# Optimization experiments

Measured on AMD Instinct MI355X. Metric: run time of the kernel, lower is better.

Reference implementation:

```python
import jax, jax.numpy as jnp
import numpy as np

B, L_PREM, T_HYP, D = 32, 256, 128, 256


def setup_inputs() -> dict:
    key = jax.random.key(0)
    ks = jax.random.split(key, 6)
    scale = 1.0 / np.sqrt(D)
    return {
        "x": jax.random.normal(ks[0], (B, L_PREM + T_HYP, D), dtype=jnp.float32),
        "w_y": jax.random.normal(ks[1], (D, D), dtype=jnp.float32) * scale,
        "w_h": jax.random.normal(ks[2], (D, D), dtype=jnp.float32) * scale,
        "w_r": jax.random.normal(ks[3], (D, D), dtype=jnp.float32) * scale,
        "w_alpha": jax.random.normal(ks[4], (D, 1), dtype=jnp.float32) * scale,
        "w_t": jax.random.normal(ks[5], (D, D), dtype=jnp.float32) * scale,
        "L": L_PREM,
    }


def reference(x, w_y, w_h, w_r, w_alpha, w_t, L):
    # x: (B, L + T, D)
    premise = x[:, :L, :]                 # Y: (B, L, D)
    hypothesis = jnp.swapaxes(x[:, L:, :], 0, 1)  # (T, B, D)

    # Y @ W_y does not depend on t: hoist out of the scan (same math).
    WY = jnp.einsum("bld,de->ble", premise, w_y)  # (B, L, D)

    def step(r_tm1, h_t):
        # r_tm1: (B, D), h_t: (B, D)
        s = h_t @ w_h + r_tm1 @ w_r                 # (B, D)
        Mt = jnp.tanh(WY + s[:, None, :])           # (B, L, D)
        scores = jnp.squeeze(Mt @ w_alpha, -1)      # (B, L)
        alpha = jax.nn.softmax(scores, axis=-1)     # (B, L)
        r_t = jnp.einsum("bl,bld->bd", alpha, premise) + r_tm1 @ w_t
        return r_t, r_t

    r0 = jnp.zeros_like(premise[:, 0, :])           # (B, D)
    _, rs = jax.lax.scan(step, r0, hypothesis)      # rs: (T, B, D)
    return jnp.swapaxes(rs, 0, 1)                   # (B, T, D)
```

## Files before the change

kernel.cpp:

```cpp
#include <hip/hip_runtime.h>
#include <hip/hip_fp16.h>

typedef unsigned long long u64;

#define C2X 2.8853900817779268f
#define LOG2E 1.4426950408889634f

#define WYS_OFF   0u
#define PR_OFF    4194304u
#define PREMH_OFF 8388608u
#define HWH_OFF   12582912u
#define WTH_OFF   16777216u
#define WTR_OFF   16908288u
#define ZP_OFF    17039360u
#define RCH_OFF   18087936u
#define MEMSET_SZ 1179648u

#define PRC_OFF   0u
#define WTRC_OFF  16384u
#define PREMC_OFF 32768u
#define WTC_OFF   49152u
#define WYC_OFF   65536u
#define HWHC_OFF  81920u
#define SCH_OFF   98304u
#define WACH_OFF  98432u
#define AL_OFF    98560u
#define RB_OFF    99584u
#define PART_OFF  100608u
#define RED_OFF   104832u
#define LDS_TOTAL 104864u

__global__ __launch_bounds__(256) void prep_all(const float* __restrict__ x,
                                                const float* __restrict__ wy,
                                                const float* __restrict__ wh,
                                                const float* __restrict__ wr,
                                                const float* __restrict__ wt,
                                                __half* __restrict__ wys,
                                                __half* __restrict__ prh,
                                                float* __restrict__ hwh,
                                                __half* __restrict__ wtrh,
                                                __half* __restrict__ premh,
                                                __half* __restrict__ wth) {
    const int blk = blockIdx.x;
    if (blk >= 1568) {
        int i = (blk - 1568) * 256 + threadIdx.x;
        float4 v; __half* dst; int e;
        if (i < 524288) {
            e = i * 4; int b = e >> 16;
            v = *(const float4*)(x + (size_t)e + (size_t)b * 32768);
            dst = premh + e;
        } else if (i < 540672) {
            e = (i - 524288) * 4;
            v = *(const float4*)(wt + e);
            dst = wth + e;
        } else return;
        __half h[4] = {__float2half(v.x),__float2half(v.y),__float2half(v.z),__float2half(v.w)};
        *(uint2*)dst = *(const uint2*)h;
        return;
    }
    __shared__ float At[8][256];
    const int d = threadIdx.x;
    int mode, row0;
    if (blk < 1024)      { mode = 0; row0 = blk * 8; }
    else if (blk < 1536) { mode = 1; row0 = (blk - 1024) * 8; }
    else                 { mode = 2; row0 = (blk - 1536) * 8; }
    for (int rr = 0; rr < 8; ++rr) {
        int r = row0 + rr;
        const float* src;
        if (mode == 0)      { int b = r >> 8, l = r & 255; src = x + (size_t)(b * 384 + l) * 256; }
        else if (mode == 1) { int tt = r >> 5, bb = r & 31; src = x + (size_t)(bb * 384 + 256 + tt) * 256; }
        else                { src = wt + (size_t)r * 256; }
        At[rr][d] = src[d];
    }
    __syncthreads();
    if (mode == 0) {
        float accy[8] = {0,0,0,0,0,0,0,0}, accr[8] = {0,0,0,0,0,0,0,0};
        for (int k = 0; k < 256; k += 2) {
            float y0 = wy[(size_t)k * 256 + d], y1 = wy[(size_t)(k + 1) * 256 + d];
            float r0 = wr[(size_t)k * 256 + d], r1 = wr[(size_t)(k + 1) * 256 + d];
#pragma unroll
            for (int rr = 0; rr < 8; ++rr) {
                float2 a = *(const float2*)&At[rr][k];
                accy[rr] = fmaf(a.x, y0, accy[rr]); accy[rr] = fmaf(a.y, y1, accy[rr]);
                accr[rr] = fmaf(a.x, r0, accr[rr]); accr[rr] = fmaf(a.y, r1, accr[rr]);
            }
        }
        for (int rr = 0; rr < 8; ++rr) {
            int r = row0 + rr;
            wys[(size_t)r * 256 + d] = __float2half(accy[rr] * C2X);
            prh[(size_t)r * 256 + d] = __float2half(accr[rr]);
        }
    } else {
        const float* w = (mode == 1) ? wh : wr;
        float acc[8] = {0,0,0,0,0,0,0,0};
        for (int k = 0; k < 256; k += 4) {
            float w0 = w[(size_t)k * 256 + d], w1 = w[(size_t)(k+1) * 256 + d];
            float w2 = w[(size_t)(k+2) * 256 + d], w3 = w[(size_t)(k+3) * 256 + d];
#pragma unroll
            for (int rr = 0; rr < 8; ++rr) {
                float4 a = *(const float4*)&At[rr][k];
                float t0 = fmaf(a.x, w0, acc[rr]);
                t0 = fmaf(a.y, w1, t0);
                t0 = fmaf(a.z, w2, t0);
                acc[rr] = fmaf(a.w, w3, t0);
            }
        }
        for (int rr = 0; rr < 8; ++rr) {
            int r = row0 + rr;
            if (mode == 1) hwh[(size_t)r * 256 + d] = acc[rr] * C2X;
            else           wtrh[(size_t)r * 256 + d] = __float2half(acc[rr]);
        }
    }
}

__device__ __forceinline__ u64 agent_load64(const u64* p) {
    return __hip_atomic_load(p, __ATOMIC_RELAXED, __HIP_MEMORY_SCOPE_AGENT);
}
__device__ __forceinline__ void agent_store64(u64* p, u64 v) {
    __hip_atomic_store(p, v, __ATOMIC_RELAXED, __HIP_MEMORY_SCOPE_AGENT);
}

__global__ __launch_bounds__(512, 1) void wbw_main(
    const __half* __restrict__ wys, const __half* __restrict__ prh,
    const __half* __restrict__ premh, const __half* __restrict__ wth,
    const __half* __restrict__ wtrh, const float* __restrict__ hwh,
    const float* __restrict__ walpha, float* __restrict__ out,
    u64* __restrict__ zp, u64* __restrict__ rch)
{
    extern __shared__ char lds[];
    const int tid = threadIdx.x;
    const int b = blockIdx.x >> 3, j = blockIdx.x & 7;

    float* hwhc  = (float*)(lds + HWHC_OFF);
    float* s_ch  = (float*)(lds + SCH_OFF);
    float* wa_ch = (float*)(lds + WACH_OFF);
    float* al    = (float*)(lds + AL_OFF);
    float* rb    = (float*)(lds + RB_OFF);
    float* part  = (float*)(lds + PART_OFF);
    float* red   = (float*)(lds + RED_OFF);

    {
        const int prt = tid & 3;
        for (int it = 0; it < 2; ++it) {
            int row = it * 128 + (tid >> 2);
            size_t g = (size_t)row * 256 + j * 32 + prt * 8;
            unsigned lo = (unsigned)row * 64 + (unsigned)prt * 16;
            *(uint4*)(lds + PRC_OFF   + lo) = *(const uint4*)(prh   + (size_t)b * 65536 + g);
            *(uint4*)(lds + WTRC_OFF  + lo) = *(const uint4*)(wtrh  + g);
            *(uint4*)(lds + PREMC_OFF + lo) = *(const uint4*)(premh + (size_t)b * 65536 + g);
            *(uint4*)(lds + WTC_OFF   + lo) = *(const uint4*)(wth   + g);
            *(uint4*)(lds + WYC_OFF   + lo) = *(const uint4*)(wys   + (size_t)b * 65536 + g);
        }
    }
    for (int it = 0; it < 8; ++it) {
        int idx = it * 512 + tid;
        int tt = idx >> 5, dd = idx & 31;
        hwhc[idx] = hwh[((size_t)tt * 32 + b) * 256 + j * 32 + dd];
    }
    if (tid < 32) wa_ch[tid] = walpha[j * 32 + tid] * (-2.0f * LOG2E);
    if (tid < 256) { al[tid] = 0.f; rb[tid] = 0.f; }
    if (tid < 8)   red[tid] = (tid == 0 || tid == 4) ? 1.f : 0.f;
    __syncthreads();

    for (int t = 0; t <= 128; ++t) {
        const int par = t & 1;
        if (t < 128) {
            {
                const int half_ = tid >> 8;
                const int s16 = (tid >> 4) & 15;
                const int d0 = (tid & 15) * 2;
                const __half* mat = (const __half*)(lds + (half_ ? WTRC_OFF : PRC_OFF));
                const float* vec = half_ ? rb : al;
                float ax = 0.f, ay = 0.f;
#pragma unroll
                for (int i = 0; i < 16; ++i) {
                    int l = s16 + i * 16;
                    float v = vec[l];
                    float2 mf = __half22float2(*(const __half2*)&mat[l * 32 + d0]);
                    ax = fmaf(v, mf.x, ax); ay = fmaf(v, mf.y, ay);
                }
                const int row = half_ * 16 + s16;
                part[row * 33 + d0] = ax; part[row * 33 + d0 + 1] = ay;
            }
            __syncthreads();
            if (tid < 32) {
                const float* rd = red + (par ^ 1) * 4;
                float rD = __builtin_amdgcn_rcpf(rd[0] + rd[1] + rd[2] + rd[3]);
                float se = 0.f, sr = 0.f;
#pragma unroll
                for (int s2 = 0; s2 < 16; ++s2) {
                    se += part[s2 * 33 + tid];
                    sr += part[(16 + s2) * 33 + tid];
                }
                s_ch[tid] = fmaf(fmaf(se, rD, sr), C2X, hwhc[t * 32 + tid]);
            }
            __syncthreads();
            {
                const int l = tid >> 1, dh = (tid & 1) << 4;
                union { uint4 u[2]; __half h[16]; } W;
                W.u[0] = *(const uint4*)(lds + WYC_OFF + (unsigned)l * 64 + (unsigned)dh * 2);
                W.u[1] = *(const uint4*)(lds + WYC_OFF + (unsigned)l * 64 + (unsigned)dh * 2 + 16);
                float acc = 0.f;
#pragma unroll
                for (int i = 0; i < 16; ++i) {
                    float arg = __half2float(W.h[i]) + s_ch[dh + i];
                    float u = __builtin_amdgcn_rcpf(__builtin_amdgcn_exp2f(arg) + 1.f);
                    acc = fmaf(wa_ch[dh + i], u, acc);
                }
                acc += __shfl_xor(acc, 1, 64);
                if ((tid & 1) == 0) {
                    u64 pk = ((u64)(unsigned)(t + 1) << 32) | (u64)__float_as_uint(acc);
                    agent_store64(&zp[(size_t)((par * 32 + b) * 8 + j) * 256 + l], pk);
                }
            }
        }
        {
            const int half_ = tid >> 8;
            const int s16 = (tid >> 4) & 15;
            const int d0 = (tid & 15) * 2;
            const __half* mat = (const __half*)(lds + (half_ ? WTC_OFF : PREMC_OFF));
            const float* vec = half_ ? rb : al;
            float ax = 0.f, ay = 0.f;
#pragma unroll
            for (int i = 0; i < 16; ++i) {
                int l = s16 + i * 16;
                float v = vec[l];
                float2 mf = __half22float2(*(const __half2*)&mat[l * 32 + d0]);
                ax = fmaf(v, mf.x, ax); ay = fmaf(v, mf.y, ay);
            }
            const int row = half_ * 16 + s16;
            part[row * 33 + d0] = ax; part[row * 33 + d0 + 1] = ay;
        }
        __syncthreads();
        if (tid >= 448 && tid < 480) {
            const int d = tid - 448;
            const float* rd = red + (par ^ 1) * 4;
            float rD = __builtin_amdgcn_rcpf(rd[0] + rd[1] + rd[2] + rd[3]);
            float se = 0.f, sr = 0.f;
#pragma unroll
            for (int s2 = 0; s2 < 16; ++s2) {
                se += part[s2 * 33 + d];
                sr += part[(16 + s2) * 33 + d];
            }
            float rv = fmaf(se, rD, sr);
            if (t >= 1) out[((size_t)b * 128 + (t - 1)) * 256 + j * 32 + d] = rv;
            if (t < 128) {
                u64 pk = ((u64)(unsigned)t << 32) | (u64)__float_as_uint(rv);
                agent_store64(&rch[(size_t)(par * 32 + b) * 256 + j * 32 + d], pk);
            }
        } else if (tid < 256 && t < 128) {
            const u64* zb = zp + (size_t)(par * 32 + b) * 2048 + tid;
            u64 v0,v1,v2,v3,v4,v5,v6,v7; int tries = 0;
            for (;;) {
                v0 = agent_load64(zb);         v1 = agent_load64(zb + 256);
                v2 = agent_load64(zb + 512);   v3 = agent_load64(zb + 768);
                v4 = agent_load64(zb + 1024);  v5 = agent_load64(zb + 1280);
                v6 = agent_load64(zb + 1536);  v7 = agent_load64(zb + 1792);
                bool ok = ((unsigned)(v0 >> 32) > (unsigned)t) & ((unsigned)(v1 >> 32) > (unsigned)t)
                        & ((unsigned)(v2 >> 32) > (unsigned)t) & ((unsigned)(v3 >> 32) > (unsigned)t)
                        & ((unsigned)(v4 >> 32) > (unsigned)t) & ((unsigned)(v5 >> 32) > (unsigned)t)
                        & ((unsigned)(v6 >> 32) > (unsigned)t) & ((unsigned)(v7 >> 32) > (unsigned)t);
                if (__all(ok)) break;
                if (++tries > 2) __builtin_amdgcn_s_sleep(1);
            }
            float zs = __uint_as_float((unsigned)v0) + __uint_as_float((unsigned)v1)
                     + __uint_as_float((unsigned)v2) + __uint_as_float((unsigned)v3)
                     + __uint_as_float((unsigned)v4) + __uint_as_float((unsigned)v5)
                     + __uint_as_float((unsigned)v6) + __uint_as_float((unsigned)v7);
            float ee = __builtin_amdgcn_exp2f(zs);
            float sv = ee;
#pragma unroll
            for (int off = 32; off; off >>= 1) sv += __shfl_xor(sv, off, 64);
            if ((tid & 63) == 0) red[par * 4 + (tid >> 6)] = sv;
            const u64* rp = &rch[(size_t)(par * 32 + b) * 256 + tid];
            u64 rv;
            for (;;) {
                rv = agent_load64(rp);
                if (__all((unsigned)(rv >> 32) >= (unsigned)t)) break;
                __builtin_amdgcn_s_sleep(1);
            }
            rb[tid] = __uint_as_float((unsigned)rv);
            al[tid] = ee;
        }
        __syncthreads();
    }
}

extern "C" void kernel_launch(void* const* d_in, const int* in_sizes, int n_in,
                              void* d_out, int out_size, void* d_ws, size_t ws_size,
                              hipStream_t stream) {
    const float* x   = (const float*)d_in[0];
    const float* wy  = (const float*)d_in[1];
    const float* wh  = (const float*)d_in[2];
    const float* wr  = (const float*)d_in[3];
    const float* wal = (const float*)d_in[4];
    const float* wt  = (const float*)d_in[5];

    char* ws = (char*)d_ws;
    __half* wys    = (__half*)(ws + WYS_OFF);
    __half* prh    = (__half*)(ws + PR_OFF);
    __half* premh  = (__half*)(ws + PREMH_OFF);
    float*  hwh    = (float*)(ws + HWH_OFF);
    __half* wth    = (__half*)(ws + WTH_OFF);
    __half* wtrh   = (__half*)(ws + WTR_OFF);
    u64*    zp     = (u64*)(ws + ZP_OFF);
    u64*    rch    = (u64*)(ws + RCH_OFF);

    hipFuncSetAttribute((const void*)wbw_main,
                        hipFuncAttributeMaxDynamicSharedMemorySize, (int)LDS_TOTAL);

    prep_all<<<3680, 256, 0, stream>>>(x, wy, wh, wr, wt, wys, prh, hwh, wtrh, premh, wth);
    hipMemsetAsync(ws + ZP_OFF, 0, MEMSET_SZ, stream);

    wbw_main<<<256, 512, LDS_TOTAL, stream>>>(wys, prh, premh, wth, wtrh, hwh,
                                              wal, (float*)d_out, zp, rch);
}
```

Baseline: 448.8 us.

## Precompute r@W_r via premise·W_t·W_r products to shorten the recurrence critical path

Adds a second prep kernel that forms premise@(W_t@W_r) and W_t@W_r products. The main loop can then compute the next step's r@W_r contribution (Lb) together with r_t in the same pass, instead of in a separate matvec after r_t arrives. This removes one dependent matvec-and-reduction stage from each of the 128 serial steps. It also splits the exp/alpha and r-fetch waits across different thread halves, swizzles LDS layouts to avoid bank conflicts, and stores hwh as half to save LDS. The cost is extra precompute, more LDS, and extra fp16 rounding error in the composed products.

```diff
diff --git a/kernel.cpp b/kernel.cpp
--- a/kernel.cpp
+++ b/kernel.cpp
@@ -9,38 +9,44 @@
 #define WYS_OFF   0u
 #define PR_OFF    4194304u
 #define PREMH_OFF 8388608u
-#define HWH_OFF   12582912u
-#define WTH_OFF   16777216u
-#define WTR_OFF   16908288u
-#define ZP_OFF    17039360u
-#define RCH_OFF   18087936u
+#define PR2_OFF   12582912u
+#define HWH_OFF   16777216u
+#define WTH_OFF   18874368u
+#define WTR2_OFF  19005440u
+#define ZP_OFF    19136512u
+#define RCH_OFF   20185088u
 #define MEMSET_SZ 1179648u
 
-#define PRC_OFF   0u
-#define WTRC_OFF  16384u
-#define PREMC_OFF 32768u
-#define WTC_OFF   49152u
-#define WYC_OFF   65536u
-#define HWHC_OFF  81920u
-#define SCH_OFF   98304u
-#define WACH_OFF  98432u
-#define AL_OFF    98560u
-#define RB_OFF    99584u
-#define PART_OFF  100608u
-#define RED_OFF   104832u
-#define LDS_TOTAL 104864u
-
-__global__ __launch_bounds__(256) void prep_all(const float* __restrict__ x,
-                                                const float* __restrict__ wy,
-                                                const float* __restrict__ wh,
-                                                const float* __restrict__ wr,
-                                                const float* __restrict__ wt,
-                                                __half* __restrict__ wys,
-                                                __half* __restrict__ prh,
-                                                float* __restrict__ hwh,
-                                                __half* __restrict__ wtrh,
-                                                __half* __restrict__ premh,
-                                                __half* __restrict__ wth) {
+#define PRC_OFF    0u
+#define WYC_OFF    16384u
+#define PREMC_OFF  32768u
+#define WTC_OFF    49152u
+#define PR2C_OFF   65536u
+#define WTR2C_OFF  81920u
+#define HWHC_OFF   98304u
+#define SCH_OFF    106496u
+#define WACH_OFF   106624u
+#define RED_OFF    106752u
+#define LBUF_OFF   106784u
+#define AL_OFF     106912u
+#define RB_OFF     108960u
+#define PART0_OFF  109984u
+#define PART1_OFF  114336u
+#define LDS_TOTAL  118688u
+
+__device__ __forceinline__ unsigned swz(unsigned o) { return o ^ ((o >> 3) & 64u); }
+
+__global__ __launch_bounds__(256) void prep_a(const float* __restrict__ x,
+                                              const float* __restrict__ wy,
+                                              const float* __restrict__ wh,
+                                              const float* __restrict__ wr,
+                                              const float* __restrict__ wt,
+                                              __half* __restrict__ wys,
+                                              __half* __restrict__ prh,
+                                              __half* __restrict__ hwhh,
+                                              float* __restrict__ wtrf,
+                                              __half* __restrict__ premh,
+                                              __half* __restrict__ wth) {
     const int blk = blockIdx.x;
     if (blk >= 1568) {
         int i = (blk - 1568) * 256 + threadIdx.x;
@@ -107,9 +113,47 @@
         }
         for (int rr = 0; rr < 8; ++rr) {
             int r = row0 + rr;
-            if (mode == 1) hwh[(size_t)r * 256 + d] = acc[rr] * C2X;
-            else           wtrh[(size_t)r * 256 + d] = __float2half(acc[rr]);
-        }
+            if (mode == 1) hwhh[(size_t)r * 256 + d] = __float2half(acc[rr] * C2X);
+            else           wtrf[(size_t)r * 256 + d] = acc[rr];
+        }
+    }
+}
+
+__global__ __launch_bounds__(256) void prep_b(const float* __restrict__ x,
+                                              const float* __restrict__ wt,
+                                              const float* __restrict__ wtrf,
+                                              __half* __restrict__ pr2h,
+                                              __half* __restrict__ wtr2h) {
+    __shared__ float At[8][256];
+    const int d = threadIdx.x;
+    const int blk = blockIdx.x;
+    const int isP = blk < 1024;
+    const int row0 = isP ? blk * 8 : (blk - 1024) * 8;
+    for (int rr = 0; rr < 8; ++rr) {
+        int r = row0 + rr;
+        const float* src;
+        if (isP) { int b = r >> 8, l = r & 255; src = x + (size_t)(b * 384 + l) * 256; }
+        else     { src = wt + (size_t)r * 256; }
+        At[rr][d] = src[d];
+    }
+    __syncthreads();
+    float acc[8] = {0,0,0,0,0,0,0,0};
+    for (int k = 0; k < 256; k += 4) {
+        float w0 = wtrf[(size_t)k * 256 + d], w1 = wtrf[(size_t)(k+1) * 256 + d];
+        float w2 = wtrf[(size_t)(k+2) * 256 + d], w3 = wtrf[(size_t)(k+3) * 256 + d];
+#pragma unroll
+        for (int rr = 0; rr < 8; ++rr) {
+            float4 a = *(const float4*)&At[rr][k];
+            float t0 = fmaf(a.x, w0, acc[rr]);
+            t0 = fmaf(a.y, w1, t0);
+            t0 = fmaf(a.z, w2, t0);
+            acc[rr] = fmaf(a.w, w3, t0);
+        }
+    }
+    for (int rr = 0; rr < 8; ++rr) {
+        int r = row0 + rr;
+        if (isP) pr2h[(size_t)r * 256 + d]  = __float2half(acc[rr]);
+        else     wtr2h[(size_t)r * 256 + d] = __float2half(acc[rr]);
     }
 }
 
@@ -123,89 +167,87 @@
 __global__ __launch_bounds__(512, 1) void wbw_main(
     const __half* __restrict__ wys, const __half* __restrict__ prh,
     const __half* __restrict__ premh, const __half* __restrict__ wth,
-    const __half* __restrict__ wtrh, const float* __restrict__ hwh,
-    const float* __restrict__ walpha, float* __restrict__ out,
-    u64* __restrict__ zp, u64* __restrict__ rch)
+    const __half* __restrict__ pr2h, const __half* __restrict__ wtr2h,
+    const __half* __restrict__ hwhh, const float* __restrict__ walpha,
+    float* __restrict__ out, u64* __restrict__ zp, u64* __restrict__ rch)
 {
     extern __shared__ char lds[];
     const int tid = threadIdx.x;
     const int b = blockIdx.x >> 3, j = blockIdx.x & 7;
 
-    float* hwhc  = (float*)(lds + HWHC_OFF);
     float* s_ch  = (float*)(lds + SCH_OFF);
     float* wa_ch = (float*)(lds + WACH_OFF);
-    float* al    = (float*)(lds + AL_OFF);
-    float* rb    = (float*)(lds + RB_OFF);
-    float* part  = (float*)(lds + PART_OFF);
-    float* red   = (float*)(lds + RED_OFF);
+    float* redb  = (float*)(lds + RED_OFF);
+    float* Lb    = (float*)(lds + LBUF_OFF);
+    float* alb   = (float*)(lds + AL_OFF);
+    float* rbb   = (float*)(lds + RB_OFF);
+    float* part0 = (float*)(lds + PART0_OFF);
+    float* part1 = (float*)(lds + PART1_OFF);
 
     {
         const int prt = tid & 3;
         for (int it = 0; it < 2; ++it) {
             int row = it * 128 + (tid >> 2);
             size_t g = (size_t)row * 256 + j * 32 + prt * 8;
-            unsigned lo = (unsigned)row * 64 + (unsigned)prt * 16;
+            unsigned lo = swz((unsigned)row * 64 + (unsigned)prt * 16);
             *(uint4*)(lds + PRC_OFF   + lo) = *(const uint4*)(prh   + (size_t)b * 65536 + g);
-            *(uint4*)(lds + WTRC_OFF  + lo) = *(const uint4*)(wtrh  + g);
+            *(uint4*)(lds + WYC_OFF   + lo) = *(const uint4*)(wys   + (size_t)b * 65536 + g);
             *(uint4*)(lds + PREMC_OFF + lo) = *(const uint4*)(premh + (size_t)b * 65536 + g);
             *(uint4*)(lds + WTC_OFF   + lo) = *(const uint4*)(wth   + g);
-            *(uint4*)(lds + WYC_OFF   + lo) = *(const uint4*)(wys   + (size_t)b * 65536 + g);
-        }
-    }
-    for (int it = 0; it < 8; ++it) {
-        int idx = it * 512 + tid;
-        int tt = idx >> 5, dd = idx & 31;
-        hwhc[idx] = hwh[((size_t)tt * 32 + b) * 256 + j * 32 + dd];
-    }
-    if (tid < 32) wa_ch[tid] = walpha[j * 32 + tid] * (-2.0f * LOG2E);
-    if (tid < 256) { al[tid] = 0.f; rb[tid] = 0.f; }
-    if (tid < 8)   red[tid] = (tid == 0 || tid == 4) ? 1.f : 0.f;
+            *(uint4*)(lds + PR2C_OFF  + lo) = *(const uint4*)(pr2h  + (size_t)b * 65536 + g);
+            *(uint4*)(lds + WTR2C_OFF + lo) = *(const uint4*)(wtr2h + g);
+        }
+    }
+    for (int it = 0; it < 2; ++it) {
+        int q4 = it * 512 + tid;
+        int tt = q4 >> 3, d4 = (q4 & 7) * 4;
+        *(uint2*)(lds + HWHC_OFF + (size_t)q4 * 8) =
+            *(const uint2*)(hwhh + ((size_t)tt * 32 + b) * 256 + j * 32 + d4);
+    }
+    if (tid < 32)  { wa_ch[tid] = walpha[j * 32 + tid] * (-2.0f * LOG2E); Lb[tid] = 0.f; }
+    if (tid < 256) { alb[tid] = 0.f; alb[256 + tid] = 0.f; rbb[tid] = 0.f; }
+    if (tid < 8)   redb[tid] = (tid == 0 || tid == 4) ? 1.f : 0.f;
     __syncthreads();
 
     for (int t = 0; t <= 128; ++t) {
-        const int par = t & 1;
+        const int par = t & 1, q = par ^ 1;
+        const float* e1 = alb + q * 256;
         if (t < 128) {
             {
-                const int half_ = tid >> 8;
-                const int s16 = (tid >> 4) & 15;
-                const int d0 = (tid & 15) * 2;
-                const __half* mat = (const __half*)(lds + (half_ ? WTRC_OFF : PRC_OFF));
-                const float* vec = half_ ? rb : al;
+                const int seg = tid >> 4, dp = tid & 15;
                 float ax = 0.f, ay = 0.f;
 #pragma unroll
-                for (int i = 0; i < 16; ++i) {
-                    int l = s16 + i * 16;
-                    float v = vec[l];
-                    float2 mf = __half22float2(*(const __half2*)&mat[l * 32 + d0]);
-                    ax = fmaf(v, mf.x, ax); ay = fmaf(v, mf.y, ay);
-                }
-                const int row = half_ * 16 + s16;
-                part[row * 33 + d0] = ax; part[row * 33 + d0 + 1] = ay;
+                for (int i = 0; i < 8; ++i) {
+                    int l = seg * 8 + i;
+                    float e = e1[l];
+                    float2 mf = __half22float2(*(const __half2*)(lds + PRC_OFF + swz((unsigned)l * 64 + (unsigned)dp * 4)));
+                    ax = fmaf(e, mf.x, ax); ay = fmaf(e, mf.y, ay);
+                }
+                *(float2*)&part0[seg * 34 + dp * 2] = make_float2(ax, ay);
             }
             __syncthreads();
             if (tid < 32) {
-                const float* rd = red + (par ^ 1) * 4;
+                const float* rd = redb + q * 4;
                 float rD = __builtin_amdgcn_rcpf(rd[0] + rd[1] + rd[2] + rd[3]);
-                float se = 0.f, sr = 0.f;
-#pragma unroll
-                for (int s2 = 0; s2 < 16; ++s2) {
-                    se += part[s2 * 33 + tid];
-                    sr += part[(16 + s2) * 33 + tid];
-                }
-                s_ch[tid] = fmaf(fmaf(se, rD, sr), C2X, hwhc[t * 32 + tid]);
+                float se = 0.f;
+#pragma unroll
+                for (int s = 0; s < 32; ++s) se += part0[s * 34 + tid];
+                float sv = fmaf(se, rD, Lb[tid]);
+                s_ch[tid] = fmaf(sv, C2X,
+                    __half2float(*(const __half*)(lds + HWHC_OFF + (size_t)(t * 32 + tid) * 2)));
             }
             __syncthreads();
             {
                 const int l = tid >> 1, dh = (tid & 1) << 4;
                 union { uint4 u[2]; __half h[16]; } W;
-                W.u[0] = *(const uint4*)(lds + WYC_OFF + (unsigned)l * 64 + (unsigned)dh * 2);
-                W.u[1] = *(const uint4*)(lds + WYC_OFF + (unsigned)l * 64 + (unsigned)dh * 2 + 16);
+                W.u[0] = *(const uint4*)(lds + WYC_OFF + swz((unsigned)l * 64 + (unsigned)dh * 2));
+                W.u[1] = *(const uint4*)(lds + WYC_OFF + swz((unsigned)l * 64 + (unsigned)dh * 2 + 16));
                 float acc = 0.f;
 #pragma unroll
                 for (int i = 0; i < 16; ++i) {
                     float arg = __half2float(W.h[i]) + s_ch[dh + i];
-                    float u = __builtin_amdgcn_rcpf(__builtin_amdgcn_exp2f(arg) + 1.f);
-                    acc = fmaf(wa_ch[dh + i], u, acc);
+                    acc = fmaf(wa_ch[dh + i],
+                               __builtin_amdgcn_rcpf(__builtin_amdgcn_exp2f(arg) + 1.f), acc);
                 }
                 acc += __shfl_xor(acc, 1, 64);
                 if ((tid & 1) == 0) {
@@ -215,40 +257,51 @@
             }
         }
         {
-            const int half_ = tid >> 8;
-            const int s16 = (tid >> 4) & 15;
-            const int d0 = (tid & 15) * 2;
-            const __half* mat = (const __half*)(lds + (half_ ? WTC_OFF : PREMC_OFF));
-            const float* vec = half_ ? rb : al;
-            float ax = 0.f, ay = 0.f;
-#pragma unroll
-            for (int i = 0; i < 16; ++i) {
-                int l = s16 + i * 16;
-                float v = vec[l];
-                float2 mf = __half22float2(*(const __half2*)&mat[l * 32 + d0]);
-                ax = fmaf(v, mf.x, ax); ay = fmaf(v, mf.y, ay);
-            }
-            const int row = half_ * 16 + s16;
-            part[row * 33 + d0] = ax; part[row * 33 + d0 + 1] = ay;
+            const int seg = tid >> 4, dp = tid & 15;
+            const float* rd = redb + q * 4;
+            float rD = __builtin_amdgcn_rcpf(rd[0] + rd[1] + rd[2] + rd[3]);
+            float rx = 0.f, ry = 0.f, lx = 0.f, ly = 0.f;
+#pragma unroll
+            for (int i = 0; i < 8; ++i) {
+                int l = seg * 8 + i;
+                float a = e1[l] * rD;
+                float r = rbb[l];
+                unsigned o = swz((unsigned)l * 64 + (unsigned)dp * 4);
+                float2 mp = __half22float2(*(const __half2*)(lds + PREMC_OFF + o));
+                float2 mt = __half22float2(*(const __half2*)(lds + WTC_OFF + o));
+                rx = fmaf(a, mp.x, rx); ry = fmaf(a, mp.y, ry);
+                rx = fmaf(r, mt.x, rx); ry = fmaf(r, mt.y, ry);
+                if (t < 128) {
+                    float2 m2 = __half22float2(*(const __half2*)(lds + PR2C_OFF + o));
+                    float2 m3 = __half22float2(*(const __half2*)(lds + WTR2C_OFF + o));
+                    lx = fmaf(a, m2.x, lx); ly = fmaf(a, m2.y, ly);
+                    lx = fmaf(r, m3.x, lx); ly = fmaf(r, m3.y, ly);
+                }
+            }
+            *(float2*)&part0[seg * 34 + dp * 2] = make_float2(rx, ry);
+            if (t < 128) *(float2*)&part1[seg * 34 + dp * 2] = make_float2(lx, ly);
         }
         __syncthreads();
-        if (tid >= 448 && tid < 480) {
-            const int d = tid - 448;
-            const float* rd = red + (par ^ 1) * 4;
-            float rD = __builtin_amdgcn_rcpf(rd[0] + rd[1] + rd[2] + rd[3]);
-            float se = 0.f, sr = 0.f;
-#pragma unroll
-            for (int s2 = 0; s2 < 16; ++s2) {
-                se += part[s2 * 33 + d];
-                sr += part[(16 + s2) * 33 + d];
-            }
-            float rv = fmaf(se, rD, sr);
-            if (t >= 1) out[((size_t)b * 128 + (t - 1)) * 256 + j * 32 + d] = rv;
-            if (t < 128) {
-                u64 pk = ((u64)(unsigned)t << 32) | (u64)__float_as_uint(rv);
-                agent_store64(&rch[(size_t)(par * 32 + b) * 256 + j * 32 + d], pk);
-            }
-        } else if (tid < 256 && t < 128) {
+        if (tid >= 448) {
+            int lane = tid - 448;
+            if (lane < 32) {
+                float rsum = 0.f;
+#pragma unroll
+                for (int s = 0; s < 32; ++s) rsum += part0[s * 34 + lane];
+                if (t >= 1) out[((size_t)b * 128 + (t - 1)) * 256 + j * 32 + lane] = rsum;
+                if (t < 128) {
+                    u64 pk = ((u64)(unsigned)t << 32) | (u64)__float_as_uint(rsum);
+                    agent_store64(&rch[(size_t)(par * 32 + b) * 256 + j * 32 + lane], pk);
+                }
+            } else if (t < 128) {
+                int d = lane - 32;
+                float ls = 0.f;
+#pragma unroll
+                for (int s = 0; s < 32; ++s) ls += part1[s * 34 + d];
+                Lb[d] = ls;
+            }
+        }
+        if (tid < 256 && t < 128) {
             const u64* zb = zp + (size_t)(par * 32 + b) * 2048 + tid;
             u64 v0,v1,v2,v3,v4,v5,v6,v7; int tries = 0;
             for (;;) {
@@ -271,16 +324,18 @@
             float sv = ee;
 #pragma unroll
             for (int off = 32; off; off >>= 1) sv += __shfl_xor(sv, off, 64);
-            if ((tid & 63) == 0) red[par * 4 + (tid >> 6)] = sv;
-            const u64* rp = &rch[(size_t)(par * 32 + b) * 256 + tid];
+            if ((tid & 63) == 0) redb[par * 4 + (tid >> 6)] = sv;
+            alb[par * 256 + tid] = ee;
+        }
+        if (tid >= 256 && t < 128) {
+            const u64* rp = &rch[(size_t)(par * 32 + b) * 256 + (tid - 256)];
             u64 rv;
             for (;;) {
                 rv = agent_load64(rp);
                 if (__all((unsigned)(rv >> 32) >= (unsigned)t)) break;
                 __builtin_amdgcn_s_sleep(1);
             }
-            rb[tid] = __uint_as_float((unsigned)rv);
-            al[tid] = ee;
+            rbb[tid - 256] = __uint_as_float((unsigned)rv);
         }
         __syncthreads();
     }
@@ -300,18 +355,21 @@
     __half* wys    = (__half*)(ws + WYS_OFF);
     __half* prh    = (__half*)(ws + PR_OFF);
     __half* premh  = (__half*)(ws + PREMH_OFF);
-    float*  hwh    = (float*)(ws + HWH_OFF);
+    __half* pr2h   = (__half*)(ws + PR2_OFF);
+    __half* hwhh   = (__half*)(ws + HWH_OFF);
     __half* wth    = (__half*)(ws + WTH_OFF);
-    __half* wtrh   = (__half*)(ws + WTR_OFF);
+    __half* wtr2h  = (__half*)(ws + WTR2_OFF);
+    float*  wtrf   = (float*)(ws + ZP_OFF);
     u64*    zp     = (u64*)(ws + ZP_OFF);
     u64*    rch    = (u64*)(ws + RCH_OFF);
 
     hipFuncSetAttribute((const void*)wbw_main,
                         hipFuncAttributeMaxDynamicSharedMemorySize, (int)LDS_TOTAL);
 
-    prep_all<<<3680, 256, 0, stream>>>(x, wy, wh, wr, wt, wys, prh, hwh, wtrh, premh, wth);
+    prep_a<<<3680, 256, 0, stream>>>(x, wy, wh, wr, wt, wys, prh, hwhh, wtrf, premh, wth);
+    prep_b<<<1056, 256, 0, stream>>>(x, wt, wtrf, pr2h, wtr2h);
     hipMemsetAsync(ws + ZP_OFF, 0, MEMSET_SZ, stream);
 
-    wbw_main<<<256, 512, LDS_TOTAL, stream>>>(wys, prh, premh, wth, wtrh, hwh,
-                                              wal, (float*)d_out, zp, rch);
-}
+    wbw_main<<<256, 512, LDS_TOTAL, stream>>>(wys, prh, premh, wth, pr2h, wtr2h,
+                                              hwhh, wal, (float*)d_out, zp, rch);
+}
```

Result: slower. 546.7 us (+21.8%).

## Split the r-update and alpha-gather across wave halves with double-buffered alpha

Applied to the files above, without the earlier changes.

The r_t matvec (alpha·premise plus r·W_t) now runs only on the upper 256 threads. They reduce it with shuffles and an LDS atomic counter, and the last wave to finish publishes the result. That removes one block-wide barrier per step. The lower half only waits on the remote z partials and writes exp values into a double-buffered alpha array, so the rch polling is moved off the z-waiting waves. The s-reduction also uses 64 threads with a shuffle. The trade-off is a new atomic-counter handoff plus a fence, and there is a race risk if the counter reset is not ordered before the next step.

```diff
diff --git a/kernel.cpp b/kernel.cpp
--- a/kernel.cpp
+++ b/kernel.cpp
@@ -16,19 +16,21 @@
 #define RCH_OFF   18087936u
 #define MEMSET_SZ 1179648u
 
-#define PRC_OFF   0u
-#define WTRC_OFF  16384u
-#define PREMC_OFF 32768u
-#define WTC_OFF   49152u
-#define WYC_OFF   65536u
-#define HWHC_OFF  81920u
-#define SCH_OFF   98304u
-#define WACH_OFF  98432u
-#define AL_OFF    98560u
-#define RB_OFF    99584u
-#define PART_OFF  100608u
-#define RED_OFF   104832u
-#define LDS_TOTAL 104864u
+#define PRC_OFF    0u
+#define WTRC_OFF   16384u
+#define PREMC_OFF  32768u
+#define WTC_OFF    49152u
+#define WYC_OFF    65536u
+#define HWHC_OFF   81920u
+#define SCH_OFF    98304u
+#define WACH_OFF   98432u
+#define RED_OFF    98560u
+#define ALB_OFF    98624u
+#define RBB_OFF    100672u
+#define PART_OFF   101696u
+#define RPART_OFF  105920u
+#define CTRL_OFF   106432u
+#define LDS_TOTAL  106496u
 
 __global__ __launch_bounds__(256) void prep_all(const float* __restrict__ x,
                                                 const float* __restrict__ wy,
@@ -134,10 +136,12 @@
     float* hwhc  = (float*)(lds + HWHC_OFF);
     float* s_ch  = (float*)(lds + SCH_OFF);
     float* wa_ch = (float*)(lds + WACH_OFF);
-    float* al    = (float*)(lds + AL_OFF);
-    float* rb    = (float*)(lds + RB_OFF);
+    float* redb  = (float*)(lds + RED_OFF);
+    float* alb   = (float*)(lds + ALB_OFF);
+    float* rbb   = (float*)(lds + RBB_OFF);
     float* part  = (float*)(lds + PART_OFF);
-    float* red   = (float*)(lds + RED_OFF);
+    float* rpart = (float*)(lds + RPART_OFF);
+    unsigned* ctrL = (unsigned*)(lds + CTRL_OFF);
 
     {
         const int prt = tid & 3;
@@ -157,20 +161,22 @@
         int tt = idx >> 5, dd = idx & 31;
         hwhc[idx] = hwh[((size_t)tt * 32 + b) * 256 + j * 32 + dd];
     }
-    if (tid < 32) wa_ch[tid] = walpha[j * 32 + tid] * (-2.0f * LOG2E);
-    if (tid < 256) { al[tid] = 0.f; rb[tid] = 0.f; }
-    if (tid < 8)   red[tid] = (tid == 0 || tid == 4) ? 1.f : 0.f;
+    if (tid < 32)  wa_ch[tid] = walpha[j * 32 + tid] * (-2.0f * LOG2E);
+    if (tid < 256) { alb[tid] = 0.f; alb[256 + tid] = 0.f; rbb[tid] = 0.f; }
+    if (tid < 8)   redb[tid] = (tid == 0 || tid == 4) ? 1.f : 0.f;
+    if (tid == 0)  *ctrL = 0u;
     __syncthreads();
 
     for (int t = 0; t <= 128; ++t) {
-        const int par = t & 1;
+        const int par = t & 1, q = par ^ 1;
+        const float* e1 = alb + q * 256;
         if (t < 128) {
             {
                 const int half_ = tid >> 8;
                 const int s16 = (tid >> 4) & 15;
                 const int d0 = (tid & 15) * 2;
                 const __half* mat = (const __half*)(lds + (half_ ? WTRC_OFF : PRC_OFF));
-                const float* vec = half_ ? rb : al;
+                const float* vec = half_ ? rbb : e1;
                 float ax = 0.f, ay = 0.f;
 #pragma unroll
                 for (int i = 0; i < 16; ++i) {
@@ -183,16 +189,18 @@
                 part[row * 33 + d0] = ax; part[row * 33 + d0 + 1] = ay;
             }
             __syncthreads();
-            if (tid < 32) {
-                const float* rd = red + (par ^ 1) * 4;
-                float rD = __builtin_amdgcn_rcpf(rd[0] + rd[1] + rd[2] + rd[3]);
-                float se = 0.f, sr = 0.f;
-#pragma unroll
-                for (int s2 = 0; s2 < 16; ++s2) {
-                    se += part[s2 * 33 + tid];
-                    sr += part[(16 + s2) * 33 + tid];
-                }
-                s_ch[tid] = fmaf(fmaf(se, rD, sr), C2X, hwhc[t * 32 + tid]);
+            if (tid < 64) {
+                const int d = tid & 31, h = tid >> 5;
+                float sum = 0.f;
+#pragma unroll
+                for (int s = 0; s < 16; ++s) sum += part[(h * 16 + s) * 33 + d];
+                float other = __shfl_xor(sum, 32, 64);
+                if (h == 0) {
+                    const float* rd = redb + q * 4;
+                    float rD = __builtin_amdgcn_rcpf(rd[0] + rd[1] + rd[2] + rd[3]);
+                    float sv = fmaf(sum, rD, other);
+                    s_ch[d] = fmaf(sv, C2X, hwhc[t * 32 + d]);
+                }
             }
             __syncthreads();
             {
@@ -204,8 +212,8 @@
 #pragma unroll
                 for (int i = 0; i < 16; ++i) {
                     float arg = __half2float(W.h[i]) + s_ch[dh + i];
-                    float u = __builtin_amdgcn_rcpf(__builtin_amdgcn_exp2f(arg) + 1.f);
-                    acc = fmaf(wa_ch[dh + i], u, acc);
+                    acc = fmaf(wa_ch[dh + i],
+                               __builtin_amdgcn_rcpf(__builtin_amdgcn_exp2f(arg) + 1.f), acc);
                 }
                 acc += __shfl_xor(acc, 1, 64);
                 if ((tid & 1) == 0) {
@@ -214,41 +222,58 @@
                 }
             }
         }
-        {
-            const int half_ = tid >> 8;
-            const int s16 = (tid >> 4) & 15;
-            const int d0 = (tid & 15) * 2;
-            const __half* mat = (const __half*)(lds + (half_ ? WTC_OFF : PREMC_OFF));
-            const float* vec = half_ ? rb : al;
+        if (tid >= 256) {
+            const int t256 = tid - 256;
+            const int lane = t256 & 63;
+            const int w    = t256 >> 6;
+            const int dp   = t256 & 15;
+            const int d0   = dp * 2;
+            const int l0   = (t256 >> 4) * 16;
+            const float* rd = redb + q * 4;
+            float rD = __builtin_amdgcn_rcpf(rd[0] + rd[1] + rd[2] + rd[3]);
             float ax = 0.f, ay = 0.f;
 #pragma unroll
             for (int i = 0; i < 16; ++i) {
-                int l = s16 + i * 16;
-                float v = vec[l];
-                float2 mf = __half22float2(*(const __half2*)&mat[l * 32 + d0]);
-                ax = fmaf(v, mf.x, ax); ay = fmaf(v, mf.y, ay);
-            }
-            const int row = half_ * 16 + s16;
-            part[row * 33 + d0] = ax; part[row * 33 + d0 + 1] = ay;
-        }
-        __syncthreads();
-        if (tid >= 448 && tid < 480) {
-            const int d = tid - 448;
-            const float* rd = red + (par ^ 1) * 4;
-            float rD = __builtin_amdgcn_rcpf(rd[0] + rd[1] + rd[2] + rd[3]);
-            float se = 0.f, sr = 0.f;
-#pragma unroll
-            for (int s2 = 0; s2 < 16; ++s2) {
-                se += part[s2 * 33 + d];
-                sr += part[(16 + s2) * 33 + d];
-            }
-            float rv = fmaf(se, rD, sr);
-            if (t >= 1) out[((size_t)b * 128 + (t - 1)) * 256 + j * 32 + d] = rv;
+                int l = l0 + i;
+                float a = e1[l] * rD;
+                float r = rbb[l];
+                unsigned o = (unsigned)l * 64 + (unsigned)d0 * 2;
+                float2 mp = __half22float2(*(const __half2*)(lds + PREMC_OFF + o));
+                float2 mt = __half22float2(*(const __half2*)(lds + WTC_OFF + o));
+                ax = fmaf(a, mp.x, ax); ax = fmaf(r, mt.x, ax);
+                ay = fmaf(a, mp.y, ay); ay = fmaf(r, mt.y, ay);
+            }
+            ax += __shfl_xor(ax, 16, 64); ax += __shfl_xor(ax, 32, 64);
+            ay += __shfl_xor(ay, 16, 64); ay += __shfl_xor(ay, 32, 64);
+            if (lane < 16) { rpart[w * 32 + d0] = ax; rpart[w * 32 + d0 + 1] = ay; }
+            __threadfence_block();
+            unsigned old = 0;
+            if (lane == 0) old = atomicAdd(ctrL, 1u);
+            old = __shfl(old, 0, 64);
+            if (old == 3u) {
+                if (lane < 32) {
+                    float rsum = rpart[lane] + rpart[32 + lane]
+                               + rpart[64 + lane] + rpart[96 + lane];
+                    if (t >= 1)
+                        out[((size_t)b * 128 + (t - 1)) * 256 + j * 32 + lane] = rsum;
+                    if (t < 128) {
+                        u64 pk = ((u64)(unsigned)t << 32) | (u64)__float_as_uint(rsum);
+                        agent_store64(&rch[(size_t)(par * 32 + b) * 256 + j * 32 + lane], pk);
+                    }
+                }
+                if (lane == 0) *ctrL = 0u;
+            }
             if (t < 128) {
-                u64 pk = ((u64)(unsigned)t << 32) | (u64)__float_as_uint(rv);
-                agent_store64(&rch[(size_t)(par * 32 + b) * 256 + j * 32 + d], pk);
-            }
-        } else if (tid < 256 && t < 128) {
+                const u64* rp = &rch[(size_t)(par * 32 + b) * 256 + t256];
+                u64 rv;
+                for (;;) {
+                    rv = agent_load64(rp);
+                    if (__all((unsigned)(rv >> 32) >= (unsigned)t)) break;
+                    __builtin_amdgcn_s_sleep(1);
+                }
+                rbb[t256] = __uint_as_float((unsigned)rv);
+            }
+        } else if (t < 128) {
             const u64* zb = zp + (size_t)(par * 32 + b) * 2048 + tid;
             u64 v0,v1,v2,v3,v4,v5,v6,v7; int tries = 0;
             for (;;) {
@@ -271,16 +296,8 @@
             float sv = ee;
 #pragma unroll
             for (int off = 32; off; off >>= 1) sv += __shfl_xor(sv, off, 64);
-            if ((tid & 63) == 0) red[par * 4 + (tid >> 6)] = sv;
-            const u64* rp = &rch[(size_t)(par * 32 + b) * 256 + tid];
-            u64 rv;
-            for (;;) {
-                rv = agent_load64(rp);
-                if (__all((unsigned)(rv >> 32) >= (unsigned)t)) break;
-                __builtin_amdgcn_s_sleep(1);
-            }
-            rb[tid] = __uint_as_float((unsigned)rv);
-            al[tid] = ee;
+            if ((tid & 63) == 0) redb[par * 4 + (tid >> 6)] = sv;
+            alb[par * 256 + tid] = ee;
         }
         __syncthreads();
     }
```

Result: slower. 497.9 us (+10.9%).
